# Optimization experiments

Hardware: AMD Instinct MI355X
Metric: run time of the kernel (lower is better)

Reference implementation:

```python
import jax, jax.numpy as jnp
import numpy as np

B, S, D = 16, 4096, 1024

def setup_inputs() -> dict:
    key = jax.random.key(0)
    k1, k2, k3, k4 = jax.random.split(key, 4)
    values = jax.random.normal(k1, (B, S, D), dtype=jnp.float32)
    contexts = jax.random.normal(k2, (B, D), dtype=jnp.float32)
    W = jax.random.normal(k3, (D, D), dtype=jnp.float32) / np.sqrt(D)
    b = jax.random.normal(k4, (D,), dtype=jnp.float32) * 0.01
    return {"values": values, "contexts": contexts, "W": W, "b": b}

def reference(values, contexts, W, b):
    # proj = values @ W^T + b  (torch nn.Linear convention with W as [out,in];
    # here W is [D,D], use x @ W.T)
    proj = jnp.einsum('bsd,ed->bse', values, W) + b  # [B,S,D]
    # single-query scores: contexts [B,D] dot proj [B,S,D] -> [B,S]
    scores = jnp.einsum('bd,bsd->bs', contexts, proj)
    attn = jax.nn.softmax(scores, axis=-1)  # [B,S]
    # weighted sum over values -> [B,D]
    return jnp.einsum('bs,bsd->bd', attn, values)
```

## Files before the change

kernel.cpp:

```cpp
#include <hip/hip_runtime.h>
#include <cstdint>
#include <cstddef>

#define BD 16
#define SD 4096
#define DD 1024
#define L2E 1.4426950408889634f
#define PREC 1028
#define NCHUNK 64

typedef float f32x4 __attribute__((ext_vector_type(4)));

__device__ __forceinline__ float dot4(f32x4 a, f32x4 b) {
    return fmaf(a.x, b.x, fmaf(a.y, b.y, fmaf(a.z, b.z, a.w * b.w)));
}

__global__ __launch_bounds__(256)
void ctx_proj_kernel(const float* __restrict__ ctx,
                     const float* __restrict__ W,
                     float* __restrict__ ctil) {
    const int tid = threadIdx.x;
    const int dl  = tid & 63;
    const int eg  = tid >> 6;
    const int dt  = blockIdx.x;
    const int b   = blockIdx.y;
    const int ez  = blockIdx.z;
    const int d4  = dt * 256 + dl * 4;

    __shared__ float cs[256];
    cs[tid] = ctx[b * DD + ez * 256 + tid];
    __syncthreads();

    f32x4 acc = {0.f, 0.f, 0.f, 0.f};
    const float* cp = cs + eg * 64;
    const float* Wp = W + (size_t)(ez * 256 + eg * 64) * DD + d4;
#pragma unroll 8
    for (int e = 0; e < 64; ++e) {
        f32x4 w = *(const f32x4*)(Wp + (size_t)e * DD);
        acc += cp[e] * w;
    }

    __shared__ f32x4 red[256];
    red[tid] = acc;
    __syncthreads();
    if (tid < 64) {
        f32x4 r = red[tid] + red[64 + tid] + red[128 + tid] + red[192 + tid];
        float* dst = ctil + b * DD + d4;
        atomicAdd(dst + 0, r.x);
        atomicAdd(dst + 1, r.y);
        atomicAdd(dst + 2, r.z);
        atomicAdd(dst + 3, r.w);
    }
}

__global__ __launch_bounds__(256)
void flash_kernel(const float* __restrict__ values,
                  const float* __restrict__ ctil,
                  float* __restrict__ partials) {
    constexpr int ROWS = SD / NCHUNK;
    const int chunk = blockIdx.x;
    const int b     = blockIdx.y;
    const int r0    = chunk * ROWS;
    const int tid   = threadIdx.x;
    const int wave  = tid >> 6;
    const int lane  = tid & 63;

    const f32x4* ct4 = (const f32x4*)(ctil + (size_t)b * DD);
    const f32x4 c0 = ct4[lane];
    const f32x4 c1 = ct4[64 + lane];
    const f32x4 c2 = ct4[128 + lane];
    const f32x4 c3 = ct4[192 + lane];

    f32x4 o0 = {0.f, 0.f, 0.f, 0.f}, o1 = o0, o2 = o0, o3 = o0;
    float m = -1e30f, l = 0.f;

#pragma unroll 2
    for (int i = wave; i < ROWS; i += 4) {
        const f32x4* v4 = (const f32x4*)(values + ((size_t)b * SD + r0 + i) * DD);
        f32x4 v0 = __builtin_nontemporal_load(v4 + lane);
        f32x4 v1 = __builtin_nontemporal_load(v4 + 64 + lane);
        f32x4 v2 = __builtin_nontemporal_load(v4 + 128 + lane);
        f32x4 v3 = __builtin_nontemporal_load(v4 + 192 + lane);

        float s = dot4(v0, c0) + dot4(v1, c1) + dot4(v2, c2) + dot4(v3, c3);
#pragma unroll
        for (int off = 32; off > 0; off >>= 1) s += __shfl_xor(s, off, 64);

        if (s > m) {
            float corr = exp2f((m - s) * L2E);
            m = s;
            l *= corr;
            o0 *= corr; o1 *= corr; o2 *= corr; o3 *= corr;
        }
        float p = exp2f((s - m) * L2E);
        l += p;
        o0 += p * v0; o1 += p * v1; o2 += p * v2; o3 += p * v3;
    }

    __shared__ float red_m[4];
    __shared__ float red_l[4];
    __shared__ f32x4 obuf[4][256];

    if (lane == 0) { red_m[wave] = m; red_l[wave] = l; }
    __syncthreads();

    const float M = fmaxf(fmaxf(red_m[0], red_m[1]), fmaxf(red_m[2], red_m[3]));
    const float Lb =
        red_l[0] * exp2f((red_m[0] - M) * L2E) +
        red_l[1] * exp2f((red_m[1] - M) * L2E) +
        red_l[2] * exp2f((red_m[2] - M) * L2E) +
        red_l[3] * exp2f((red_m[3] - M) * L2E);

    const float corr = exp2f((m - M) * L2E);
    o0 *= corr; o1 *= corr; o2 *= corr; o3 *= corr;

    obuf[wave][lane]       = o0;
    obuf[wave][64 + lane]  = o1;
    obuf[wave][128 + lane] = o2;
    obuf[wave][192 + lane] = o3;
    __syncthreads();

    f32x4 t = obuf[0][tid] + obuf[1][tid] + obuf[2][tid] + obuf[3][tid];

    float* part = partials + (size_t)(b * NCHUNK + chunk) * PREC;
    ((f32x4*)part)[tid] = t;
    if (tid == 0) { part[1024] = M; part[1025] = Lb; }
}

__global__ __launch_bounds__(256)
void finalize_kernel(const float* __restrict__ partials,
                     float* __restrict__ out) {
    const int dt  = blockIdx.x;
    const int b   = blockIdx.y;
    const int tid = threadIdx.x;
    const float* base = partials + (size_t)b * NCHUNK * PREC;

    __shared__ float corr_s[NCHUNK];
    __shared__ float L_s;

    if (tid < 64) {
        const int lane = tid;
        float mv = base[(size_t)lane * PREC + 1024];
        float lv = base[(size_t)lane * PREC + 1025];
        float mm = mv;
#pragma unroll
        for (int off = 32; off > 0; off >>= 1) mm = fmaxf(mm, __shfl_xor(mm, off, 64));
        float c = exp2f((mv - mm) * L2E);
        corr_s[lane] = c;
        float lp = c * lv;
#pragma unroll
        for (int off = 32; off > 0; off >>= 1) lp += __shfl_xor(lp, off, 64);
        if (lane == 0) L_s = lp;
    }
    __syncthreads();

    const float inv = 1.0f / L_s;
    const int d = dt * 256 + tid;
    float acc = 0.f;
#pragma unroll 16
    for (int i = 0; i < NCHUNK; ++i)
        acc = fmaf(corr_s[i], base[(size_t)i * PREC + d], acc);
    out[(size_t)b * DD + d] = acc * inv;
}

extern "C" void kernel_launch(void* const* d_in, const int* in_sizes, int n_in,
                              void* d_out, int out_size, void* d_ws, size_t ws_size,
                              hipStream_t stream) {
    const float* values = (const float*)d_in[0];
    const float* ctx    = (const float*)d_in[1];
    const float* W      = (const float*)d_in[2];
    float* out = (float*)d_out;

    float* ctil     = (float*)d_ws;
    float* partials = ctil + (size_t)BD * DD;

    hipMemsetAsync(ctil, 0, (size_t)BD * DD * sizeof(float), stream);
    ctx_proj_kernel<<<dim3(4, BD, 4), 256, 0, stream>>>(ctx, W, ctil);
    flash_kernel<<<dim3(NCHUNK, BD), 256, 0, stream>>>(values, ctil, partials);
    finalize_kernel<<<dim3(4, BD), 256, 0, stream>>>(partials, out);
}
```

Baseline: 60.99 us.

## Fuse finalize into flash kernel, drop memset/atomics, prefetch value rows

The atomic accumulation of the context projection is replaced by per-slice partial outputs that the flash kernel sums on load, which removes the memset launch. The finalize kernel is folded into the flash kernel using a last-block-done counter per batch, removing one launch. The flash loop now software-prefetches the next row and uses a branchless online-softmax update. Together these cut launch overhead and hide memory latency, at the cost of extra exp2 work per row and a serialized tail reduction in one block per batch.

```diff
diff --git a/kernel.cpp b/kernel.cpp
--- a/kernel.cpp
+++ b/kernel.cpp
@@ -15,10 +15,12 @@
     return fmaf(a.x, b.x, fmaf(a.y, b.y, fmaf(a.z, b.z, a.w * b.w)));
 }
 
+
 __global__ __launch_bounds__(256)
 void ctx_proj_kernel(const float* __restrict__ ctx,
                      const float* __restrict__ W,
-                     float* __restrict__ ctil) {
+                     float* __restrict__ ctilp,
+                     int* __restrict__ cnt) {
     const int tid = threadIdx.x;
     const int dl  = tid & 63;
     const int eg  = tid >> 6;
@@ -26,6 +28,8 @@
     const int b   = blockIdx.y;
     const int ez  = blockIdx.z;
     const int d4  = dt * 256 + dl * 4;
+
+    if (dt == 0 && ez == 0 && tid == 0) cnt[b] = 0;
 
     __shared__ float cs[256];
     cs[tid] = ctx[b * DD + ez * 256 + tid];
@@ -35,28 +39,24 @@
     const float* cp = cs + eg * 64;
     const float* Wp = W + (size_t)(ez * 256 + eg * 64) * DD + d4;
 #pragma unroll 8
-    for (int e = 0; e < 64; ++e) {
-        f32x4 w = *(const f32x4*)(Wp + (size_t)e * DD);
-        acc += cp[e] * w;
-    }
+    for (int e = 0; e < 64; ++e)
+        acc += cp[e] * *(const f32x4*)(Wp + (size_t)e * DD);
 
     __shared__ f32x4 red[256];
     red[tid] = acc;
     __syncthreads();
     if (tid < 64) {
         f32x4 r = red[tid] + red[64 + tid] + red[128 + tid] + red[192 + tid];
-        float* dst = ctil + b * DD + d4;
-        atomicAdd(dst + 0, r.x);
-        atomicAdd(dst + 1, r.y);
-        atomicAdd(dst + 2, r.z);
-        atomicAdd(dst + 3, r.w);
+        *(f32x4*)(ctilp + (size_t)(b * 4 + ez) * DD + d4) = r;
     }
 }
 
 __global__ __launch_bounds__(256)
 void flash_kernel(const float* __restrict__ values,
-                  const float* __restrict__ ctil,
-                  float* __restrict__ partials) {
+                  const float* __restrict__ ctilp,
+                  float* __restrict__ partials,
+                  int* __restrict__ cnt,
+                  float* __restrict__ out) {
     constexpr int ROWS = SD / NCHUNK;
     const int chunk = blockIdx.x;
     const int b     = blockIdx.y;
@@ -65,37 +65,51 @@
     const int wave  = tid >> 6;
     const int lane  = tid & 63;
 
-    const f32x4* ct4 = (const f32x4*)(ctil + (size_t)b * DD);
-    const f32x4 c0 = ct4[lane];
-    const f32x4 c1 = ct4[64 + lane];
-    const f32x4 c2 = ct4[128 + lane];
-    const f32x4 c3 = ct4[192 + lane];
+    const f32x4* cp0 = (const f32x4*)(ctilp + (size_t)(b * 4 + 0) * DD);
+    const f32x4* cp1 = (const f32x4*)(ctilp + (size_t)(b * 4 + 1) * DD);
+    const f32x4* cp2 = (const f32x4*)(ctilp + (size_t)(b * 4 + 2) * DD);
+    const f32x4* cp3 = (const f32x4*)(ctilp + (size_t)(b * 4 + 3) * DD);
+    const f32x4 c0 = cp0[lane]       + cp1[lane]       + cp2[lane]       + cp3[lane];
+    const f32x4 c1 = cp0[64 + lane]  + cp1[64 + lane]  + cp2[64 + lane]  + cp3[64 + lane];
+    const f32x4 c2 = cp0[128 + lane] + cp1[128 + lane] + cp2[128 + lane] + cp3[128 + lane];
+    const f32x4 c3 = cp0[192 + lane] + cp1[192 + lane] + cp2[192 + lane] + cp3[192 + lane];
 
     f32x4 o0 = {0.f, 0.f, 0.f, 0.f}, o1 = o0, o2 = o0, o3 = o0;
     float m = -1e30f, l = 0.f;
 
-#pragma unroll 2
-    for (int i = wave; i < ROWS; i += 4) {
-        const f32x4* v4 = (const f32x4*)(values + ((size_t)b * SD + r0 + i) * DD);
-        f32x4 v0 = __builtin_nontemporal_load(v4 + lane);
-        f32x4 v1 = __builtin_nontemporal_load(v4 + 64 + lane);
-        f32x4 v2 = __builtin_nontemporal_load(v4 + 128 + lane);
-        f32x4 v3 = __builtin_nontemporal_load(v4 + 192 + lane);
+    const f32x4* vb = (const f32x4*)(values + ((size_t)b * SD + r0) * DD);
 
-        float s = dot4(v0, c0) + dot4(v1, c1) + dot4(v2, c2) + dot4(v3, c3);
-#pragma unroll
-        for (int off = 32; off > 0; off >>= 1) s += __shfl_xor(s, off, 64);
+#define ACCUM(v0, v1, v2, v3) do {                                          \
+    float s_ = dot4(v0, c0) + dot4(v1, c1) + dot4(v2, c2) + dot4(v3, c3);   \
+    _Pragma("unroll")                                                       \
+    for (int off_ = 32; off_ > 0; off_ >>= 1) s_ += __shfl_xor(s_, off_, 64); \
+    float mn_   = fmaxf(m, s_);                                             \
+    float corr_ = exp2f((m - mn_) * L2E);                                   \
+    float pw_   = exp2f((s_ - mn_) * L2E);                                  \
+    m = mn_;                                                                \
+    l = fmaf(l, corr_, pw_);                                                \
+    o0 = o0 * corr_ + pw_ * v0;  o1 = o1 * corr_ + pw_ * v1;                \
+    o2 = o2 * corr_ + pw_ * v2;  o3 = o3 * corr_ + pw_ * v3;                \
+} while (0)
 
-        if (s > m) {
-            float corr = exp2f((m - s) * L2E);
-            m = s;
-            l *= corr;
-            o0 *= corr; o1 *= corr; o2 *= corr; o3 *= corr;
-        }
-        float p = exp2f((s - m) * L2E);
-        l += p;
-        o0 += p * v0; o1 += p * v1; o2 += p * v2; o3 += p * v3;
+    const f32x4* p0 = vb + (size_t)wave * (DD / 4);
+    f32x4 va0 = __builtin_nontemporal_load(p0 + lane);
+    f32x4 va1 = __builtin_nontemporal_load(p0 + 64 + lane);
+    f32x4 va2 = __builtin_nontemporal_load(p0 + 128 + lane);
+    f32x4 va3 = __builtin_nontemporal_load(p0 + 192 + lane);
+
+#pragma unroll 1
+    for (int i = wave + 4; i < ROWS; i += 4) {
+        const f32x4* q = vb + (size_t)i * (DD / 4);
+        f32x4 n0 = __builtin_nontemporal_load(q + lane);
+        f32x4 n1 = __builtin_nontemporal_load(q + 64 + lane);
+        f32x4 n2 = __builtin_nontemporal_load(q + 128 + lane);
+        f32x4 n3 = __builtin_nontemporal_load(q + 192 + lane);
+        ACCUM(va0, va1, va2, va3);
+        va0 = n0; va1 = n1; va2 = n2; va3 = n3;
     }
+    ACCUM(va0, va1, va2, va3);
+#undef ACCUM
 
     __shared__ float red_m[4];
     __shared__ float red_l[4];
@@ -112,12 +126,10 @@
         red_l[3] * exp2f((red_m[3] - M) * L2E);
 
     const float corr = exp2f((m - M) * L2E);
-    o0 *= corr; o1 *= corr; o2 *= corr; o3 *= corr;
-
-    obuf[wave][lane]       = o0;
-    obuf[wave][64 + lane]  = o1;
-    obuf[wave][128 + lane] = o2;
-    obuf[wave][192 + lane] = o3;
+    obuf[wave][lane]       = o0 * corr;
+    obuf[wave][64 + lane]  = o1 * corr;
+    obuf[wave][128 + lane] = o2 * corr;
+    obuf[wave][192 + lane] = o3 * corr;
     __syncthreads();
 
     f32x4 t = obuf[0][tid] + obuf[1][tid] + obuf[2][tid] + obuf[3][tid];
@@ -125,42 +137,40 @@
     float* part = partials + (size_t)(b * NCHUNK + chunk) * PREC;
     ((f32x4*)part)[tid] = t;
     if (tid == 0) { part[1024] = M; part[1025] = Lb; }
-}
 
-__global__ __launch_bounds__(256)
-void finalize_kernel(const float* __restrict__ partials,
-                     float* __restrict__ out) {
-    const int dt  = blockIdx.x;
-    const int b   = blockIdx.y;
-    const int tid = threadIdx.x;
+    __shared__ int amLast;
+    __threadfence();
+    __syncthreads();
+    if (tid == 0) amLast = (atomicAdd(&cnt[b], 1) == NCHUNK - 1);
+    __syncthreads();
+    if (!amLast) return;
+    __threadfence();
+
     const float* base = partials + (size_t)b * NCHUNK * PREC;
-
     __shared__ float corr_s[NCHUNK];
     __shared__ float L_s;
 
     if (tid < 64) {
-        const int lane = tid;
-        float mv = base[(size_t)lane * PREC + 1024];
-        float lv = base[(size_t)lane * PREC + 1025];
+        float mv = base[(size_t)tid * PREC + 1024];
+        float lv = base[(size_t)tid * PREC + 1025];
         float mm = mv;
 #pragma unroll
         for (int off = 32; off > 0; off >>= 1) mm = fmaxf(mm, __shfl_xor(mm, off, 64));
         float c = exp2f((mv - mm) * L2E);
-        corr_s[lane] = c;
+        corr_s[tid] = c;
         float lp = c * lv;
 #pragma unroll
         for (int off = 32; off > 0; off >>= 1) lp += __shfl_xor(lp, off, 64);
-        if (lane == 0) L_s = lp;
+        if (tid == 0) L_s = lp;
     }
     __syncthreads();
 
     const float inv = 1.0f / L_s;
-    const int d = dt * 256 + tid;
-    float acc = 0.f;
-#pragma unroll 16
+    f32x4 acc = {0.f, 0.f, 0.f, 0.f};
+#pragma unroll 8
     for (int i = 0; i < NCHUNK; ++i)
-        acc = fmaf(corr_s[i], base[(size_t)i * PREC + d], acc);
-    out[(size_t)b * DD + d] = acc * inv;
+        acc += corr_s[i] * *(const f32x4*)(base + (size_t)i * PREC + tid * 4);
+    *(f32x4*)(out + (size_t)b * DD + tid * 4) = acc * inv;
 }
 
 extern "C" void kernel_launch(void* const* d_in, const int* in_sizes, int n_in,
@@ -171,11 +181,10 @@
     const float* W      = (const float*)d_in[2];
     float* out = (float*)d_out;
 
-    float* ctil     = (float*)d_ws;
-    float* partials = ctil + (size_t)BD * DD;
+    int*   cnt      = (int*)d_ws;
+    float* ctilp    = (float*)d_ws + 16;
+    float* partials = ctilp + (size_t)BD * 4 * DD;
 
-    hipMemsetAsync(ctil, 0, (size_t)BD * DD * sizeof(float), stream);
-    ctx_proj_kernel<<<dim3(4, BD, 4), 256, 0, stream>>>(ctx, W, ctil);
-    flash_kernel<<<dim3(NCHUNK, BD), 256, 0, stream>>>(values, ctil, partials);
-    finalize_kernel<<<dim3(4, BD), 256, 0, stream>>>(partials, out);
+    ctx_proj_kernel<<<dim3(4, BD, 4), 256, 0, stream>>>(ctx, W, ctilp, cnt);
+    flash_kernel<<<dim3(NCHUNK, BD), 256, 0, stream>>>(values, ctilp, partials, cnt, out);
 }
```

Result: slower. 224.2 us (+267.6%).
